# Optimization experiments

Hardware: AMD Instinct MI355X
Metric: run time of the kernel (lower is better)

Reference implementation:

```python
import jax, jax.numpy as jnp
import numpy as np

N = 100000
E = 1200000
F_IN = 128
HID = 32
HEADS = 4
OUT_HEADS = 1
N_CLASSES = 40
NEG_SLOPE = 0.2


def _glorot(key, shape):
    fan_in, fan_out = shape[0], shape[-1]
    lim = jnp.sqrt(6.0 / (fan_in + fan_out))
    return jax.random.uniform(key, shape, jnp.float32, -lim, lim)


def setup_inputs() -> dict:
    key = jax.random.key(0)
    ks = jax.random.split(key, 16)
    x = jax.random.normal(ks[0], (N, F_IN), jnp.float32)
    edge_index = jax.random.randint(ks[1], (2, E), 0, N, jnp.int32)
    # layer 0: F_IN -> HID per head, HEADS heads, concat
    W0 = _glorot(ks[2], (F_IN, HEADS * HID))
    a_src0 = _glorot(ks[3], (HEADS, HID))
    a_dst0 = _glorot(ks[4], (HEADS, HID))
    b0 = jnp.zeros((HEADS * HID,), jnp.float32)
    # layer 1: HEADS*HID -> HID per head, HEADS heads, concat
    W1 = _glorot(ks[5], (HEADS * HID, HEADS * HID))
    a_src1 = _glorot(ks[6], (HEADS, HID))
    a_dst1 = _glorot(ks[7], (HEADS, HID))
    b1 = jnp.zeros((HEADS * HID,), jnp.float32)
    # layer 2: HEADS*HID -> N_CLASSES, OUT_HEADS heads, concat=False (mean)
    W2 = _glorot(ks[8], (HEADS * HID, OUT_HEADS * N_CLASSES))
    a_src2 = _glorot(ks[9], (OUT_HEADS, N_CLASSES))
    a_dst2 = _glorot(ks[10], (OUT_HEADS, N_CLASSES))
    b2 = jnp.zeros((N_CLASSES,), jnp.float32)
    return dict(x=x, edge_index=edge_index,
                W0=W0, a_src0=a_src0, a_dst0=a_dst0, b0=b0,
                W1=W1, a_src1=a_src1, a_dst1=a_dst1, b1=b1,
                W2=W2, a_src2=a_src2, a_dst2=a_dst2, b2=b2)


def gat_conv(x, src, dst, W, a_src, a_dst, b, heads, ch, concat):
    n = x.shape[0]
    h = (x @ W).reshape(n, heads, ch)                      # [N,H,C]
    # per-node attention logits for source/target roles
    s_src = jnp.einsum('nhc,hc->nh', h, a_src)             # [N,H]
    s_dst = jnp.einsum('nhc,hc->nh', h, a_dst)             # [N,H]
    e = jax.nn.leaky_relu(s_src[src] + s_dst[dst], NEG_SLOPE)  # [E,H]
    # segment softmax over incoming edges of each target node
    emax = jax.ops.segment_max(e, dst, num_segments=n)
    ex = jnp.exp(e - emax[dst])
    denom = jax.ops.segment_sum(ex, dst, num_segments=n)
    alpha = ex / (denom[dst] + 1e-16)                       # [E,H]
    msg = h[src] * alpha[:, :, None]                        # [E,H,C]
    out = jax.ops.segment_sum(msg, dst, num_segments=n)     # [N,H,C]
    out = out.reshape(n, heads * ch) if concat else out.mean(axis=1)
    return out + b


def reference(x, edge_index, W0, a_src0, a_dst0, b0, W1, a_src1, a_dst1, b1,
              W2, a_src2, a_dst2, b2):
    # add self loops (PyG GATConv default)
    loops = jnp.arange(N, dtype=edge_index.dtype)
    src = jnp.concatenate([edge_index[0], loops])
    dst = jnp.concatenate([edge_index[1], loops])
    h = jax.nn.elu(gat_conv(x, src, dst, W0, a_src0, a_dst0, b0, HEADS, HID, True))
    h = jax.nn.elu(gat_conv(h, src, dst, W1, a_src1, a_dst1, b1, HEADS, HID, True))
    h = gat_conv(h, src, dst, W2, a_src2, a_dst2, b2, OUT_HEADS, N_CLASSES, False)
    return jax.nn.log_softmax(h, axis=1)
```

## Files before the change

kernel.cpp:

```cpp
#include <hip/hip_runtime.h>
#include <hip/hip_bf16.h>

#define FIN   128
#define HEADS 4
#define HID   32
#define NCLS  40
#define NEG_SLOPE 0.2f

#define BKT_SH 10
#define BKT    1024
#define NB_MAX 128
#define TILE_E 8192

typedef __bf16 bf16x8 __attribute__((ext_vector_type(8)));
typedef float  f32x4  __attribute__((ext_vector_type(4)));

__device__ inline unsigned short bf16_rne(float f) {
    unsigned u = __float_as_uint(f);
    return (unsigned short)((u + 0x7fffu + ((u >> 16) & 1u)) >> 16);
}
__device__ inline float bf16_to_f(unsigned short h) {
    return __uint_as_float(((unsigned)h) << 16);
}

__device__ inline void packW_dev(const float* __restrict__ W, unsigned short* __restrict__ Bhi,
                                 unsigned short* __restrict__ Blo, int NO, int NC, int idx) {
    int i = idx & 7;
    int rest = idx >> 3;
    int l = rest & 63;
    int rest2 = rest >> 6;
    int c = rest2 % NC;
    int t = rest2 / NC;
    int k   = t * 32 + (l >> 4) * 8 + i;
    int col = c * 16 + (l & 15);
    float val = (col < NO) ? W[(size_t)k * NO + col] : 0.f;
    unsigned short hi = bf16_rne(val);
    unsigned short lo = bf16_rne(val - bf16_to_f(hi));
    Bhi[idx] = hi;
    Blo[idx] = lo;
}

__device__ inline void packS_dev(const float* __restrict__ W, const float* __restrict__ asrc,
                                 const float* __restrict__ adst, unsigned short* __restrict__ Shi,
                                 unsigned short* __restrict__ Slo, int NO, int HH, int CH, int idx) {
    int i = idx & 7;
    int l = (idx >> 3) & 63;
    int t = idx >> 9;
    int k = t * 32 + (l >> 4) * 8 + i;
    int j = l & 15;
    float val = 0.f;
    if (j < 2 * HH) {
        int h = (j < HH) ? j : j - HH;
        const float* av = (j < HH) ? (asrc + h * CH) : (adst + h * CH);
        const float* wr = W + (size_t)k * NO + h * CH;
        for (int c = 0; c < CH; ++c) val += wr[c] * av[c];
    }
    unsigned short hi = bf16_rne(val);
    unsigned short lo = bf16_rne(val - bf16_to_f(hi));
    Shi[idx] = hi;
    Slo[idx] = lo;
}

__global__ __launch_bounds__(256) void packAll_k(
        const float* __restrict__ W0, const float* __restrict__ W1, const float* __restrict__ W2,
        const float* __restrict__ as0, const float* __restrict__ ad0,
        const float* __restrict__ as1, const float* __restrict__ ad1,
        const float* __restrict__ as2, const float* __restrict__ ad2,
        unsigned short* __restrict__ Bhi0, unsigned short* __restrict__ Blo0,
        unsigned short* __restrict__ Bhi1, unsigned short* __restrict__ Blo1,
        unsigned short* __restrict__ Bhi2, unsigned short* __restrict__ Blo2,
        unsigned short* __restrict__ Shi0, unsigned short* __restrict__ Slo0,
        unsigned short* __restrict__ Shi1, unsigned short* __restrict__ Slo1,
        unsigned short* __restrict__ Shi2, unsigned short* __restrict__ Slo2,
        int* __restrict__ cnt1) {
    int gid = blockIdx.x * 256 + threadIdx.x;
    if      (gid < 16384) packW_dev(W0, Bhi0, Blo0, 128, 8, gid);
    else if (gid < 32768) packW_dev(W1, Bhi1, Blo1, 128, 8, gid - 16384);
    else if (gid < 38912) packW_dev(W2, Bhi2, Blo2, NCLS, 3, gid - 32768);
    else if (gid < 40960) packS_dev(W0, as0, ad0, Shi0, Slo0, 128, 4, HID, gid - 38912);
    else if (gid < 43008) packS_dev(W1, as1, ad1, Shi1, Slo1, 128, 4, HID, gid - 40960);
    else if (gid < 45056) packS_dev(W2, as2, ad2, Shi2, Slo2, NCLS, 1, NCLS, gid - 43008);
    else if (gid < 45056 + NB_MAX) cnt1[gid - 45056] = 0;
}

template<int NC, int HH>
__global__ __launch_bounds__(256) void gemm_fused_k(
        const float* __restrict__ X, const unsigned short* __restrict__ Bhi,
        const unsigned short* __restrict__ Blo, const unsigned short* __restrict__ Shi,
        const unsigned short* __restrict__ Slo, unsigned short* __restrict__ Hbf,
        float* __restrict__ ssrc, float* __restrict__ sdst, int n, int NO) {
    int wave = threadIdx.x >> 6;
    int lane = threadIdx.x & 63;
    int rowbase = (blockIdx.x * 4 + wave) * 32;
    if (rowbase >= n) return;
    int r0 = lane & 15, kg = lane >> 4;

    f32x4 acc[2][NC];
    f32x4 accS[2];
#pragma unroll
    for (int rt = 0; rt < 2; ++rt) {
        accS[rt] = f32x4{0.f, 0.f, 0.f, 0.f};
#pragma unroll
        for (int c = 0; c < NC; ++c) acc[rt][c] = f32x4{0.f, 0.f, 0.f, 0.f};
    }

    for (int t = 0; t < 4; ++t) {
        union U { unsigned short u[8]; bf16x8 v; };
        U ah[2], al[2];
#pragma unroll
        for (int rt = 0; rt < 2; ++rt) {
            int row = min(rowbase + rt * 16 + r0, n - 1);
            const float* xp = X + (size_t)row * 128 + t * 32 + kg * 8;
            float4 xa = *reinterpret_cast<const float4*>(xp);
            float4 xb = *reinterpret_cast<const float4*>(xp + 4);
            float f[8] = {xa.x, xa.y, xa.z, xa.w, xb.x, xb.y, xb.z, xb.w};
#pragma unroll
            for (int i = 0; i < 8; ++i) {
                unsigned short h = bf16_rne(f[i]);
                ah[rt].u[i] = h;
                al[rt].u[i] = bf16_rne(f[i] - bf16_to_f(h));
            }
        }
#pragma unroll
        for (int c = 0; c < NC; ++c) {
            size_t boff = (((size_t)t * NC + c) * 64 + lane) * 8;
            bf16x8 bh = *reinterpret_cast<const bf16x8*>(Bhi + boff);
            bf16x8 bl = *reinterpret_cast<const bf16x8*>(Blo + boff);
#pragma unroll
            for (int rt = 0; rt < 2; ++rt) {
                acc[rt][c] = __builtin_amdgcn_mfma_f32_16x16x32_bf16(ah[rt].v, bh, acc[rt][c], 0, 0, 0);
                acc[rt][c] = __builtin_amdgcn_mfma_f32_16x16x32_bf16(al[rt].v, bh, acc[rt][c], 0, 0, 0);
                acc[rt][c] = __builtin_amdgcn_mfma_f32_16x16x32_bf16(ah[rt].v, bl, acc[rt][c], 0, 0, 0);
            }
        }
        {
            size_t soff = ((size_t)t * 64 + lane) * 8;
            bf16x8 sh = *reinterpret_cast<const bf16x8*>(Shi + soff);
            bf16x8 sl = *reinterpret_cast<const bf16x8*>(Slo + soff);
#pragma unroll
            for (int rt = 0; rt < 2; ++rt) {
                accS[rt] = __builtin_amdgcn_mfma_f32_16x16x32_bf16(ah[rt].v, sh, accS[rt], 0, 0, 0);
                accS[rt] = __builtin_amdgcn_mfma_f32_16x16x32_bf16(al[rt].v, sh, accS[rt], 0, 0, 0);
                accS[rt] = __builtin_amdgcn_mfma_f32_16x16x32_bf16(ah[rt].v, sl, accS[rt], 0, 0, 0);
            }
        }
    }

#pragma unroll
    for (int rt = 0; rt < 2; ++rt)
#pragma unroll
        for (int r = 0; r < 4; ++r) {
            int row = rowbase + rt * 16 + kg * 4 + r;
            if (row >= n) continue;
            if (HH == 4) {
                if (r0 < 4)      ssrc[(size_t)row * 4 + r0]       = accS[rt][r];
                else if (r0 < 8) sdst[(size_t)row * 4 + (r0 - 4)] = accS[rt][r];
            } else {
                if (r0 == 0)      ssrc[row] = accS[rt][r];
                else if (r0 == 1) sdst[row] = accS[rt][r];
            }
#pragma unroll
            for (int c = 0; c < NC; ++c) {
                int col = c * 16 + r0;
                if (col < NO)
                    Hbf[(size_t)row * NO + col] = bf16_rne(acc[rt][c][r]);
            }
        }
}

template<int NC, int HH, int OSTRIDE>
__global__ __launch_bounds__(256) void gemm_bf16s_k(
        const unsigned short* __restrict__ Xbf, const unsigned short* __restrict__ Bhi,
        const unsigned short* __restrict__ Blo, const unsigned short* __restrict__ Shi,
        const unsigned short* __restrict__ Slo, unsigned short* __restrict__ Hbf,
        float* __restrict__ ssrc, float* __restrict__ sdst, int n, int NO) {
    int wave = threadIdx.x >> 6;
    int lane = threadIdx.x & 63;
    int rowbase = (blockIdx.x * 4 + wave) * 32;
    if (rowbase >= n) return;
    int r0 = lane & 15, kg = lane >> 4;

    f32x4 acc[2][NC];
    f32x4 accS[2];
#pragma unroll
    for (int rt = 0; rt < 2; ++rt) {
        accS[rt] = f32x4{0.f, 0.f, 0.f, 0.f};
#pragma unroll
        for (int c = 0; c < NC; ++c) acc[rt][c] = f32x4{0.f, 0.f, 0.f, 0.f};
    }

    for (int t = 0; t < 4; ++t) {
        bf16x8 av[2];
#pragma unroll
        for (int rt = 0; rt < 2; ++rt) {
            int row = min(rowbase + rt * 16 + r0, n - 1);
            av[rt] = *reinterpret_cast<const bf16x8*>(Xbf + (size_t)row * 128 + t * 32 + kg * 8);
        }
#pragma unroll
        for (int c = 0; c < NC; ++c) {
            size_t boff = (((size_t)t * NC + c) * 64 + lane) * 8;
            bf16x8 bh = *reinterpret_cast<const bf16x8*>(Bhi + boff);
            bf16x8 bl = *reinterpret_cast<const bf16x8*>(Blo + boff);
#pragma unroll
            for (int rt = 0; rt < 2; ++rt) {
                acc[rt][c] = __builtin_amdgcn_mfma_f32_16x16x32_bf16(av[rt], bh, acc[rt][c], 0, 0, 0);
                acc[rt][c] = __builtin_amdgcn_mfma_f32_16x16x32_bf16(av[rt], bl, acc[rt][c], 0, 0, 0);
            }
        }
        {
            size_t soff = ((size_t)t * 64 + lane) * 8;
            bf16x8 sh = *reinterpret_cast<const bf16x8*>(Shi + soff);
            bf16x8 sl = *reinterpret_cast<const bf16x8*>(Slo + soff);
#pragma unroll
            for (int rt = 0; rt < 2; ++rt) {
                accS[rt] = __builtin_amdgcn_mfma_f32_16x16x32_bf16(av[rt], sh, accS[rt], 0, 0, 0);
                accS[rt] = __builtin_amdgcn_mfma_f32_16x16x32_bf16(av[rt], sl, accS[rt], 0, 0, 0);
            }
        }
    }

#pragma unroll
    for (int rt = 0; rt < 2; ++rt)
#pragma unroll
        for (int r = 0; r < 4; ++r) {
            int row = rowbase + rt * 16 + kg * 4 + r;
            if (row >= n) continue;
            if (HH == 4) {
                if (r0 < 4)      ssrc[(size_t)row * 4 + r0]       = accS[rt][r];
                else if (r0 < 8) sdst[(size_t)row * 4 + (r0 - 4)] = accS[rt][r];
            } else {
                if (r0 == 0)      ssrc[row] = accS[rt][r];
                else if (r0 == 1) sdst[row] = accS[rt][r];
            }
#pragma unroll
            for (int c = 0; c < NC; ++c) {
                int col = c * 16 + r0;
                if (col < NO)
                    Hbf[(size_t)row * OSTRIDE + col] = bf16_rne(acc[rt][c][r]);
            }
        }
}

__global__ __launch_bounds__(256) void histA_k(const int* __restrict__ ei, int E, int Etot,
                                               int nb, int* __restrict__ cnt1) {
    __shared__ int h[NB_MAX];
    for (int i = threadIdx.x; i < nb; i += 256) h[i] = 0;
    __syncthreads();
    int base = blockIdx.x * TILE_E;
    int lim = min(base + TILE_E, Etot);
    for (int e = base + threadIdx.x; e < lim; e += 256) {
        int d = (e < E) ? ei[E + e] : e - E;
        atomicAdd(&h[d >> BKT_SH], 1);
    }
    __syncthreads();
    for (int i = threadIdx.x; i < nb; i += 256)
        if (h[i]) atomicAdd(&cnt1[i], h[i]);
}

__global__ void scanB_k(const int* __restrict__ cnt1, int* __restrict__ bbase,
                        int* __restrict__ gcur1, int nb) {
    __shared__ int tmp[128];
    int l = threadIdx.x;
    int v = (l < nb) ? cnt1[l] : 0;
    tmp[l] = v;
    __syncthreads();
    for (int off = 1; off < 128; off <<= 1) {
        int t = (l >= off) ? tmp[l - off] : 0;
        __syncthreads();
        tmp[l] += t;
        __syncthreads();
    }
    if (l < nb) { int ex = tmp[l] - v; bbase[l] = ex; gcur1[l] = ex; }
    if (l == 0) bbase[nb] = tmp[127];
}

__global__ __launch_bounds__(256) void placeA_k(const int* __restrict__ ei, int E, int Etot,
                                                int nb, int* __restrict__ gcur1,
                                                unsigned* __restrict__ pairs) {
    __shared__ int h[NB_MAX];
    __shared__ int cur[NB_MAX];
    for (int i = threadIdx.x; i < nb; i += 256) h[i] = 0;
    __syncthreads();
    int base = blockIdx.x * TILE_E;
    int lim = min(base + TILE_E, Etot);
    for (int e = base + threadIdx.x; e < lim; e += 256) {
        int d = (e < E) ? ei[E + e] : e - E;
        atomicAdd(&h[d >> BKT_SH], 1);
    }
    __syncthreads();
    for (int i = threadIdx.x; i < nb; i += 256)
        cur[i] = h[i] ? atomicAdd(&gcur1[i], h[i]) : 0;
    __syncthreads();
    for (int e = base + threadIdx.x; e < lim; e += 256) {
        int s, d;
        if (e < E) { s = ei[e]; d = ei[E + e]; } else { s = d = e - E; }
        int p = atomicAdd(&cur[d >> BKT_SH], 1);
        pairs[p] = ((unsigned)s << BKT_SH) | (unsigned)(d & (BKT - 1));
    }
}

__global__ __launch_bounds__(256) void buildcsr_k(const unsigned* __restrict__ pairs,
                                                  const int* __restrict__ bbase,
                                                  int* __restrict__ rowptr,
                                                  int* __restrict__ cols,
                                                  int n, int etot) {
    __shared__ int cnt[BKT];
    __shared__ int part[256];
    int b = blockIdx.x;
    int d0 = b << BKT_SH;
    int nd = min(BKT, n - d0);
    int rbeg = bbase[b], rend = bbase[b + 1];
    for (int i = threadIdx.x; i < nd; i += 256) cnt[i] = 0;
    __syncthreads();
    for (int i = rbeg + threadIdx.x; i < rend; i += 256)
        atomicAdd(&cnt[pairs[i] & (BKT - 1)], 1);
    __syncthreads();

    int t = threadIdx.x;
    int i4 = t * 4;
    int myv[4];
    int s0 = 0;
#pragma unroll
    for (int j = 0; j < 4; ++j) { myv[j] = (i4 + j < nd) ? cnt[i4 + j] : 0; s0 += myv[j]; }
    part[t] = s0;
    __syncthreads();
    for (int off = 1; off < 256; off <<= 1) {
        int tv = (t >= off) ? part[t - off] : 0;
        __syncthreads();
        part[t] += tv;
        __syncthreads();
    }
    int run = rbeg + part[t] - s0;
#pragma unroll
    for (int j = 0; j < 4; ++j) {
        if (i4 + j < nd) {
            rowptr[d0 + i4 + j] = run;
            cnt[i4 + j] = run;
            run += myv[j];
        }
    }
    if (b == 0 && t == 0) rowptr[n] = etot;
    __syncthreads();
    for (int i = rbeg + threadIdx.x; i < rend; i += 256) {
        unsigned p = pairs[i];
        int pos = atomicAdd(&cnt[p & (BKT - 1)], 1);
        cols[pos] = (int)(p >> BKT_SH);
    }
}

__global__ __launch_bounds__(256) void gat128_k(
        const int* __restrict__ rp, const int* __restrict__ cols,
        const unsigned short* __restrict__ Hbf, const float* __restrict__ ssrc,
        const float* __restrict__ sdst, const float* __restrict__ bias,
        unsigned short* __restrict__ outbf, int n) {
    int d = (blockIdx.x * 256 + threadIdx.x) >> 4;
    if (d >= n) return;
    int l = threadIdx.x & 15;
    int head = l >> 2;
    int sub  = l & 3;
    int beg = rp[d], end = rp[d + 1];

    float sdh = sdst[(size_t)d * 4 + head];

    float m = -1e30f, den = 0.f;
    for (int i = beg + sub; i < end; i += 4) {
        int s = cols[i];
        float v = ssrc[(size_t)s * 4 + head] + sdh;
        v = (v >= 0.f) ? v : NEG_SLOPE * v;
        float nm = fmaxf(m, v);
        den = den * __expf(m - nm) + __expf(v - nm);
        m = nm;
    }
#pragma unroll
    for (int off = 1; off <= 2; off <<= 1) {
        float om = __shfl_xor(m, off, 64);
        float od = __shfl_xor(den, off, 64);
        float nm = fmaxf(m, om);
        den = den * __expf(m - nm) + od * __expf(om - nm);
        m = nm;
    }
    float r = 1.f / (den + 1e-16f);

    float4 a0 = {0.f, 0.f, 0.f, 0.f}, a1 = {0.f, 0.f, 0.f, 0.f};
    float4 c0 = {0.f, 0.f, 0.f, 0.f}, c1 = {0.f, 0.f, 0.f, 0.f};

    auto proc = [&](int i, float4& p0, float4& p1) {
        int s = cols[i];
        float v = ssrc[(size_t)s * 4 + head] + sdh;
        v = (v >= 0.f) ? v : NEG_SLOPE * v;
        float a = __expf(v - m);
        const unsigned short* hp = Hbf + (size_t)s * 128 + l * 8;
        uint4 q = *reinterpret_cast<const uint4*>(hp);
        p0.x += a * __uint_as_float(q.x << 16);
        p0.y += a * __uint_as_float(q.x & 0xffff0000u);
        p0.z += a * __uint_as_float(q.y << 16);
        p0.w += a * __uint_as_float(q.y & 0xffff0000u);
        p1.x += a * __uint_as_float(q.z << 16);
        p1.y += a * __uint_as_float(q.z & 0xffff0000u);
        p1.z += a * __uint_as_float(q.w << 16);
        p1.w += a * __uint_as_float(q.w & 0xffff0000u);
    };

    int i = beg;
    int rem = (end - beg) & 3;
    if (rem & 1) { proc(i, a0, a1); ++i; }
    if (rem & 2) { proc(i, a0, a1); proc(i + 1, c0, c1); i += 2; }
    for (; i < end; i += 4) {
        int s0 = cols[i], s1 = cols[i + 1], s2 = cols[i + 2], s3 = cols[i + 3];
        float w0 = ssrc[(size_t)s0 * 4 + head] + sdh;
        float w1 = ssrc[(size_t)s1 * 4 + head] + sdh;
        float w2 = ssrc[(size_t)s2 * 4 + head] + sdh;
        float w3 = ssrc[(size_t)s3 * 4 + head] + sdh;
        uint4 q0 = *reinterpret_cast<const uint4*>(Hbf + (size_t)s0 * 128 + l * 8);
        uint4 q1 = *reinterpret_cast<const uint4*>(Hbf + (size_t)s1 * 128 + l * 8);
        uint4 q2 = *reinterpret_cast<const uint4*>(Hbf + (size_t)s2 * 128 + l * 8);
        uint4 q3 = *reinterpret_cast<const uint4*>(Hbf + (size_t)s3 * 128 + l * 8);
        w0 = (w0 >= 0.f) ? w0 : NEG_SLOPE * w0;
        w1 = (w1 >= 0.f) ? w1 : NEG_SLOPE * w1;
        w2 = (w2 >= 0.f) ? w2 : NEG_SLOPE * w2;
        w3 = (w3 >= 0.f) ? w3 : NEG_SLOPE * w3;
        float e0 = __expf(w0 - m), e1 = __expf(w1 - m);
        float e2 = __expf(w2 - m), e3 = __expf(w3 - m);
        a0.x += e0 * __uint_as_float(q0.x << 16);
        a0.y += e0 * __uint_as_float(q0.x & 0xffff0000u);
        a0.z += e0 * __uint_as_float(q0.y << 16);
        a0.w += e0 * __uint_as_float(q0.y & 0xffff0000u);
        a1.x += e0 * __uint_as_float(q0.z << 16);
        a1.y += e0 * __uint_as_float(q0.z & 0xffff0000u);
        a1.z += e0 * __uint_as_float(q0.w << 16);
        a1.w += e0 * __uint_as_float(q0.w & 0xffff0000u);
        c0.x += e1 * __uint_as_float(q1.x << 16);
        c0.y += e1 * __uint_as_float(q1.x & 0xffff0000u);
        c0.z += e1 * __uint_as_float(q1.y << 16);
        c0.w += e1 * __uint_as_float(q1.y & 0xffff0000u);
        c1.x += e1 * __uint_as_float(q1.z << 16);
        c1.y += e1 * __uint_as_float(q1.z & 0xffff0000u);
        c1.z += e1 * __uint_as_float(q1.w << 16);
        c1.w += e1 * __uint_as_float(q1.w & 0xffff0000u);
        a0.x += e2 * __uint_as_float(q2.x << 16);
        a0.y += e2 * __uint_as_float(q2.x & 0xffff0000u);
        a0.z += e2 * __uint_as_float(q2.y << 16);
        a0.w += e2 * __uint_as_float(q2.y & 0xffff0000u);
        a1.x += e2 * __uint_as_float(q2.z << 16);
        a1.y += e2 * __uint_as_float(q2.z & 0xffff0000u);
        a1.z += e2 * __uint_as_float(q2.w << 16);
        a1.w += e2 * __uint_as_float(q2.w & 0xffff0000u);
        c0.x += e3 * __uint_as_float(q3.x << 16);
        c0.y += e3 * __uint_as_float(q3.x & 0xffff0000u);
        c0.z += e3 * __uint_as_float(q3.y << 16);
        c0.w += e3 * __uint_as_float(q3.y & 0xffff0000u);
        c1.x += e3 * __uint_as_float(q3.z << 16);
        c1.y += e3 * __uint_as_float(q3.z & 0xffff0000u);
        c1.z += e3 * __uint_as_float(q3.w << 16);
        c1.w += e3 * __uint_as_float(q3.w & 0xffff0000u);
    }
    a0.x += c0.x; a0.y += c0.y; a0.z += c0.z; a0.w += c0.w;
    a1.x += c1.x; a1.y += c1.y; a1.z += c1.z; a1.w += c1.w;

    float4 b0 = *reinterpret_cast<const float4*>(bias + l * 8);
    float4 b1 = *reinterpret_cast<const float4*>(bias + l * 8 + 4);
    float4 v0, v1;
    v0.x = a0.x * r + b0.x; v0.y = a0.y * r + b0.y;
    v0.z = a0.z * r + b0.z; v0.w = a0.w * r + b0.w;
    v1.x = a1.x * r + b1.x; v1.y = a1.y * r + b1.y;
    v1.z = a1.z * r + b1.z; v1.w = a1.w * r + b1.w;
    v0.x = (v0.x > 0.f) ? v0.x : expm1f(v0.x);
    v0.y = (v0.y > 0.f) ? v0.y : expm1f(v0.y);
    v0.z = (v0.z > 0.f) ? v0.z : expm1f(v0.z);
    v0.w = (v0.w > 0.f) ? v0.w : expm1f(v0.w);
    v1.x = (v1.x > 0.f) ? v1.x : expm1f(v1.x);
    v1.y = (v1.y > 0.f) ? v1.y : expm1f(v1.y);
    v1.z = (v1.z > 0.f) ? v1.z : expm1f(v1.z);
    v1.w = (v1.w > 0.f) ? v1.w : expm1f(v1.w);

    uint4 u;
    u.x = (unsigned)bf16_rne(v0.x) | ((unsigned)bf16_rne(v0.y) << 16);
    u.y = (unsigned)bf16_rne(v0.z) | ((unsigned)bf16_rne(v0.w) << 16);
    u.z = (unsigned)bf16_rne(v1.x) | ((unsigned)bf16_rne(v1.y) << 16);
    u.w = (unsigned)bf16_rne(v1.z) | ((unsigned)bf16_rne(v1.w) << 16);
    *reinterpret_cast<uint4*>(outbf + (size_t)d * 128 + l * 8) = u;
}

__global__ __launch_bounds__(256) void gat40_k(
        const int* __restrict__ rp, const int* __restrict__ cols,
        const unsigned short* __restrict__ Hbf, const float* __restrict__ ssrc,
        const float* __restrict__ sdst, const float* __restrict__ b2,
        float* __restrict__ out, int n) {
    int d = (blockIdx.x * 256 + threadIdx.x) >> 4;
    if (d >= n) return;
    int l = threadIdx.x & 15;
    int beg = rp[d], end = rp[d + 1];
    float sd = sdst[d];

    float m = -1e30f, den = 0.f;
    for (int i = beg + l; i < end; i += 16) {
        int s = cols[i];
        float v = ssrc[s] + sd;
        v = (v >= 0.f) ? v : NEG_SLOPE * v;
        float nm = fmaxf(m, v);
        den = den * __expf(m - nm) + __expf(v - nm);
        m = nm;
    }
#pragma unroll
    for (int off = 1; off <= 8; off <<= 1) {
        float om = __shfl_xor(m, off, 64);
        float od = __shfl_xor(den, off, 64);
        float nm = fmaxf(m, om);
        den = den * __expf(m - nm) + od * __expf(om - nm);
        m = nm;
    }
    float r = 1.f / (den + 1e-16f);

    float4 acc = {0.f, 0.f, 0.f, 0.f};
    float4 acc2 = {0.f, 0.f, 0.f, 0.f};
    auto proc = [&](int i, float4& p) {
        int s = cols[i];
        float v = ssrc[s] + sd;
        v = (v >= 0.f) ? v : NEG_SLOPE * v;
        float a = __expf(v - m);
        uint2 q = *reinterpret_cast<const uint2*>(Hbf + (size_t)s * 64 + l * 4);
        p.x += a * __uint_as_float(q.x << 16);
        p.y += a * __uint_as_float(q.x & 0xffff0000u);
        p.z += a * __uint_as_float(q.y << 16);
        p.w += a * __uint_as_float(q.y & 0xffff0000u);
    };
    int i = beg;
    int rem = (end - beg) & 3;
    if (rem & 1) { proc(i, acc); ++i; }
    if (rem & 2) { proc(i, acc); proc(i + 1, acc2); i += 2; }
    for (; i < end; i += 4) {
        int s0 = cols[i], s1 = cols[i + 1], s2 = cols[i + 2], s3 = cols[i + 3];
        float w0 = ssrc[s0] + sd, w1 = ssrc[s1] + sd;
        float w2 = ssrc[s2] + sd, w3 = ssrc[s3] + sd;
        uint2 q0 = *reinterpret_cast<const uint2*>(Hbf + (size_t)s0 * 64 + l * 4);
        uint2 q1 = *reinterpret_cast<const uint2*>(Hbf + (size_t)s1 * 64 + l * 4);
        uint2 q2 = *reinterpret_cast<const uint2*>(Hbf + (size_t)s2 * 64 + l * 4);
        uint2 q3 = *reinterpret_cast<const uint2*>(Hbf + (size_t)s3 * 64 + l * 4);
        w0 = (w0 >= 0.f) ? w0 : NEG_SLOPE * w0;
        w1 = (w1 >= 0.f) ? w1 : NEG_SLOPE * w1;
        w2 = (w2 >= 0.f) ? w2 : NEG_SLOPE * w2;
        w3 = (w3 >= 0.f) ? w3 : NEG_SLOPE * w3;
        float e0 = __expf(w0 - m), e1 = __expf(w1 - m);
        float e2 = __expf(w2 - m), e3 = __expf(w3 - m);
        acc.x += e0 * __uint_as_float(q0.x << 16);
        acc.y += e0 * __uint_as_float(q0.x & 0xffff0000u);
        acc.z += e0 * __uint_as_float(q0.y << 16);
        acc.w += e0 * __uint_as_float(q0.y & 0xffff0000u);
        acc2.x += e1 * __uint_as_float(q1.x << 16);
        acc2.y += e1 * __uint_as_float(q1.x & 0xffff0000u);
        acc2.z += e1 * __uint_as_float(q1.y << 16);
        acc2.w += e1 * __uint_as_float(q1.y & 0xffff0000u);
        acc.x += e2 * __uint_as_float(q2.x << 16);
        acc.y += e2 * __uint_as_float(q2.x & 0xffff0000u);
        acc.z += e2 * __uint_as_float(q2.y << 16);
        acc.w += e2 * __uint_as_float(q2.y & 0xffff0000u);
        acc2.x += e3 * __uint_as_float(q3.x << 16);
        acc2.y += e3 * __uint_as_float(q3.x & 0xffff0000u);
        acc2.z += e3 * __uint_as_float(q3.y << 16);
        acc2.w += e3 * __uint_as_float(q3.y & 0xffff0000u);
    }
    acc.x += acc2.x; acc.y += acc2.y; acc.z += acc2.z; acc.w += acc2.w;

    float4 v4 = {0.f, 0.f, 0.f, 0.f};
    float mm = -1e30f;
    if (l < 10) {
        float4 b = *reinterpret_cast<const float4*>(b2 + l * 4);
        v4.x = acc.x * r + b.x; v4.y = acc.y * r + b.y;
        v4.z = acc.z * r + b.z; v4.w = acc.w * r + b.w;
        mm = fmaxf(fmaxf(v4.x, v4.y), fmaxf(v4.z, v4.w));
    }
    for (int off = 8; off > 0; off >>= 1) mm = fmaxf(mm, __shfl_xor(mm, off, 16));
    float ss = 0.f;
    if (l < 10)
        ss = __expf(v4.x - mm) + __expf(v4.y - mm) + __expf(v4.z - mm) + __expf(v4.w - mm);
    for (int off = 8; off > 0; off >>= 1) ss += __shfl_xor(ss, off, 16);
    float lse = mm + logf(ss);
    if (l < 10) {
        float4 o;
        o.x = v4.x - lse; o.y = v4.y - lse; o.z = v4.z - lse; o.w = v4.w - lse;
        *reinterpret_cast<float4*>(out + (size_t)d * 40 + l * 4) = o;
    }
}

static inline dim3 g1(long t) { return dim3((unsigned)((t + 255) / 256)); }

extern "C" void kernel_launch(void* const* d_in, const int* in_sizes, int n_in,
                              void* d_out, int out_size, void* d_ws, size_t ws_size,
                              hipStream_t stream) {
    const float* x      = (const float*)d_in[0];
    const int*   ei     = (const int*)d_in[1];
    const float* W0     = (const float*)d_in[2];
    const float* a_src0 = (const float*)d_in[3];
    const float* a_dst0 = (const float*)d_in[4];
    const float* b0     = (const float*)d_in[5];
    const float* W1     = (const float*)d_in[6];
    const float* a_src1 = (const float*)d_in[7];
    const float* a_dst1 = (const float*)d_in[8];
    const float* b1     = (const float*)d_in[9];
    const float* W2     = (const float*)d_in[10];
    const float* a_src2 = (const float*)d_in[11];
    const float* a_dst2 = (const float*)d_in[12];
    const float* b2     = (const float*)d_in[13];

    const int N    = in_sizes[0] / FIN;
    const int E    = in_sizes[1] / 2;
    const int Etot = E + N;
    const int NB   = (N + BKT - 1) / BKT;

    float* ws = (float*)d_ws;
    size_t o = 0;
    unsigned short* Hbf = (unsigned short*)(ws + o); o += (size_t)N * FIN / 2;
    unsigned short* Obf = (unsigned short*)(ws + o); o += (size_t)N * FIN / 2;
    float* ssrcA = ws + o; o += (size_t)N * HEADS;
    float* sdstA = ws + o; o += (size_t)N * HEADS;
    float* ssrcB = ws + o; o += (size_t)N * HEADS;
    float* sdstB = ws + o; o += (size_t)N * HEADS;
    int* cnt1   = (int*)(ws + o); o += NB_MAX;
    int* bbase  = (int*)(ws + o); o += NB_MAX + 2;
    int* gcur1  = (int*)(ws + o); o += NB_MAX;
    int* rowptr = (int*)(ws + o); o += N + 1;
    int* cols   = (int*)(ws + o); o += Etot;
    unsigned* pairs = (unsigned*)(ws + o); o += Etot;
    unsigned short* Bhi0 = (unsigned short*)(ws + o); o += 4 * 8 * 64 * 8 / 2;
    unsigned short* Blo0 = (unsigned short*)(ws + o); o += 4 * 8 * 64 * 8 / 2;
    unsigned short* Bhi1 = (unsigned short*)(ws + o); o += 4 * 8 * 64 * 8 / 2;
    unsigned short* Blo1 = (unsigned short*)(ws + o); o += 4 * 8 * 64 * 8 / 2;
    unsigned short* Bhi2 = (unsigned short*)(ws + o); o += 4 * 3 * 64 * 8 / 2;
    unsigned short* Blo2 = (unsigned short*)(ws + o); o += 4 * 3 * 64 * 8 / 2;
    unsigned short* Shi0 = (unsigned short*)(ws + o); o += 4 * 64 * 8 / 2;
    unsigned short* Slo0 = (unsigned short*)(ws + o); o += 4 * 64 * 8 / 2;
    unsigned short* Shi1 = (unsigned short*)(ws + o); o += 4 * 64 * 8 / 2;
    unsigned short* Slo1 = (unsigned short*)(ws + o); o += 4 * 64 * 8 / 2;
    unsigned short* Shi2 = (unsigned short*)(ws + o); o += 4 * 64 * 8 / 2;
    unsigned short* Slo2 = (unsigned short*)(ws + o); o += 4 * 64 * 8 / 2;

    const int gemmBlocks = (N + 127) / 128;
    const int grpBlocks  = (N * 16 + 255) / 256;
    const int eTiles     = (Etot + TILE_E - 1) / TILE_E;

    packAll_k<<<g1(45056 + NB_MAX), 256, 0, stream>>>(
        W0, W1, W2, a_src0, a_dst0, a_src1, a_dst1, a_src2, a_dst2,
        Bhi0, Blo0, Bhi1, Blo1, Bhi2, Blo2,
        Shi0, Slo0, Shi1, Slo1, Shi2, Slo2, cnt1);
    histA_k<<<eTiles, 256, 0, stream>>>(ei, E, Etot, NB, cnt1);
    scanB_k<<<1, 128, 0, stream>>>(cnt1, bbase, gcur1, NB);
    placeA_k<<<eTiles, 256, 0, stream>>>(ei, E, Etot, NB, gcur1, pairs);
    buildcsr_k<<<NB, 256, 0, stream>>>(pairs, bbase, rowptr, cols, N, Etot);

    gemm_fused_k<8, 4><<<gemmBlocks, 256, 0, stream>>>(x, Bhi0, Blo0, Shi0, Slo0, Hbf, ssrcA, sdstA, N, 128);
    gat128_k<<<grpBlocks, 256, 0, stream>>>(rowptr, cols, Hbf, ssrcA, sdstA, b0, Obf, N);

    gemm_bf16s_k<8, 4, 128><<<gemmBlocks, 256, 0, stream>>>(Obf, Bhi1, Blo1, Shi1, Slo1, Hbf, ssrcB, sdstB, N, 128);
    gat128_k<<<grpBlocks, 256, 0, stream>>>(rowptr, cols, Hbf, ssrcB, sdstB, b1, Obf, N);

    gemm_bf16s_k<3, 1, 64><<<gemmBlocks, 256, 0, stream>>>(Obf, Bhi2, Blo2, Shi2, Slo2, Hbf, ssrcA, sdstA, N, NCLS);
    gat40_k<<<grpBlocks, 256, 0, stream>>>(rowptr, cols, Hbf, ssrcA, sdstA, b2, (float*)d_out, N);
}
```

Baseline: 331.7 us.

## Drop softmax max pass in GAT aggregation and split layer-2 features compactly

Removes the first pass over each node's incoming edges, which computed the running max and denominator. The exponentials are now taken unshifted and the denominator is accumulated in the same loop as the weighted feature sum, so each edge list is read once instead of twice. The layer-2 projected features are also stored as a dense 32-column array plus an 8-column side array instead of a padded 64-column row, which cuts gather traffic. Skipping the max subtraction risks exp overflow or precision loss if the attention logits get large.

```diff
diff --git a/kernel.cpp b/kernel.cpp
--- a/kernel.cpp
+++ b/kernel.cpp
@@ -168,11 +168,12 @@
         }
 }
 
-template<int NC, int HH, int OSTRIDE>
+template<int NC, int HH, bool SPLIT>
 __global__ __launch_bounds__(256) void gemm_bf16s_k(
         const unsigned short* __restrict__ Xbf, const unsigned short* __restrict__ Bhi,
         const unsigned short* __restrict__ Blo, const unsigned short* __restrict__ Shi,
         const unsigned short* __restrict__ Slo, unsigned short* __restrict__ Hbf,
+        unsigned short* __restrict__ H8,
         float* __restrict__ ssrc, float* __restrict__ sdst, int n, int NO) {
     int wave = threadIdx.x >> 6;
     int lane = threadIdx.x & 63;
@@ -235,8 +236,15 @@
 #pragma unroll
             for (int c = 0; c < NC; ++c) {
                 int col = c * 16 + r0;
-                if (col < NO)
-                    Hbf[(size_t)row * OSTRIDE + col] = bf16_rne(acc[rt][c][r]);
+                if (col < NO) {
+                    unsigned short b = bf16_rne(acc[rt][c][r]);
+                    if (!SPLIT) {
+                        Hbf[(size_t)row * 128 + col] = b;
+                    } else {
+                        if (col < 32) Hbf[(size_t)row * 32 + col] = b;
+                        else          H8[(size_t)row * 8 + (col - 32)] = b;
+                    }
+                }
             }
         }
 }
@@ -357,38 +365,20 @@
     if (d >= n) return;
     int l = threadIdx.x & 15;
     int head = l >> 2;
-    int sub  = l & 3;
     int beg = rp[d], end = rp[d + 1];
 
     float sdh = sdst[(size_t)d * 4 + head];
-
-    float m = -1e30f, den = 0.f;
-    for (int i = beg + sub; i < end; i += 4) {
-        int s = cols[i];
-        float v = ssrc[(size_t)s * 4 + head] + sdh;
-        v = (v >= 0.f) ? v : NEG_SLOPE * v;
-        float nm = fmaxf(m, v);
-        den = den * __expf(m - nm) + __expf(v - nm);
-        m = nm;
-    }
-#pragma unroll
-    for (int off = 1; off <= 2; off <<= 1) {
-        float om = __shfl_xor(m, off, 64);
-        float od = __shfl_xor(den, off, 64);
-        float nm = fmaxf(m, om);
-        den = den * __expf(m - nm) + od * __expf(om - nm);
-        m = nm;
-    }
-    float r = 1.f / (den + 1e-16f);
 
     float4 a0 = {0.f, 0.f, 0.f, 0.f}, a1 = {0.f, 0.f, 0.f, 0.f};
     float4 c0 = {0.f, 0.f, 0.f, 0.f}, c1 = {0.f, 0.f, 0.f, 0.f};
+    float den = 0.f;
 
     auto proc = [&](int i, float4& p0, float4& p1) {
         int s = cols[i];
         float v = ssrc[(size_t)s * 4 + head] + sdh;
         v = (v >= 0.f) ? v : NEG_SLOPE * v;
-        float a = __expf(v - m);
+        float a = __expf(v);
+        den += a;
         const unsigned short* hp = Hbf + (size_t)s * 128 + l * 8;
         uint4 q = *reinterpret_cast<const uint4*>(hp);
         p0.x += a * __uint_as_float(q.x << 16);
@@ -419,8 +409,9 @@
         w1 = (w1 >= 0.f) ? w1 : NEG_SLOPE * w1;
         w2 = (w2 >= 0.f) ? w2 : NEG_SLOPE * w2;
         w3 = (w3 >= 0.f) ? w3 : NEG_SLOPE * w3;
-        float e0 = __expf(w0 - m), e1 = __expf(w1 - m);
-        float e2 = __expf(w2 - m), e3 = __expf(w3 - m);
+        float e0 = __expf(w0), e1 = __expf(w1);
+        float e2 = __expf(w2), e3 = __expf(w3);
+        den += e0 + e1 + e2 + e3;
         a0.x += e0 * __uint_as_float(q0.x << 16);
         a0.y += e0 * __uint_as_float(q0.x & 0xffff0000u);
         a0.z += e0 * __uint_as_float(q0.y << 16);
@@ -457,6 +448,7 @@
     a0.x += c0.x; a0.y += c0.y; a0.z += c0.z; a0.w += c0.w;
     a1.x += c1.x; a1.y += c1.y; a1.z += c1.z; a1.w += c1.w;
 
+    float r = 1.f / (den + 1e-16f);
     float4 b0 = *reinterpret_cast<const float4*>(bias + l * 8);
     float4 b1 = *reinterpret_cast<const float4*>(bias + l * 8 + 4);
     float4 v0, v1;
@@ -483,42 +475,32 @@
 
 __global__ __launch_bounds__(256) void gat40_k(
         const int* __restrict__ rp, const int* __restrict__ cols,
-        const unsigned short* __restrict__ Hbf, const float* __restrict__ ssrc,
-        const float* __restrict__ sdst, const float* __restrict__ b2,
-        float* __restrict__ out, int n) {
+        const unsigned short* __restrict__ H32, const unsigned short* __restrict__ H8,
+        const float* __restrict__ ssrc, const float* __restrict__ sdst,
+        const float* __restrict__ b2, float* __restrict__ out, int n) {
     int d = (blockIdx.x * 256 + threadIdx.x) >> 4;
     if (d >= n) return;
     int l = threadIdx.x & 15;
     int beg = rp[d], end = rp[d + 1];
     float sd = sdst[d];
 
-    float m = -1e30f, den = 0.f;
-    for (int i = beg + l; i < end; i += 16) {
-        int s = cols[i];
-        float v = ssrc[s] + sd;
-        v = (v >= 0.f) ? v : NEG_SLOPE * v;
-        float nm = fmaxf(m, v);
-        den = den * __expf(m - nm) + __expf(v - nm);
-        m = nm;
-    }
-#pragma unroll
-    for (int off = 1; off <= 8; off <<= 1) {
-        float om = __shfl_xor(m, off, 64);
-        float od = __shfl_xor(den, off, 64);
-        float nm = fmaxf(m, om);
-        den = den * __expf(m - nm) + od * __expf(om - nm);
-        m = nm;
-    }
-    float r = 1.f / (den + 1e-16f);
+    bool lo32 = (l < 8);
+    int o32 = l * 4;
+    int o8  = ((l >= 8 && l < 10) ? (l - 8) : 0) * 4;
 
     float4 acc = {0.f, 0.f, 0.f, 0.f};
     float4 acc2 = {0.f, 0.f, 0.f, 0.f};
+    float den = 0.f;
+
     auto proc = [&](int i, float4& p) {
         int s = cols[i];
         float v = ssrc[s] + sd;
         v = (v >= 0.f) ? v : NEG_SLOPE * v;
-        float a = __expf(v - m);
-        uint2 q = *reinterpret_cast<const uint2*>(Hbf + (size_t)s * 64 + l * 4);
+        float a = __expf(v);
+        den += a;
+        const unsigned short* hp = lo32 ? (H32 + (size_t)s * 32 + o32)
+                                        : (H8  + (size_t)s * 8  + o8);
+        uint2 q = *reinterpret_cast<const uint2*>(hp);
         p.x += a * __uint_as_float(q.x << 16);
         p.y += a * __uint_as_float(q.x & 0xffff0000u);
         p.z += a * __uint_as_float(q.y << 16);
@@ -532,16 +514,21 @@
         int s0 = cols[i], s1 = cols[i + 1], s2 = cols[i + 2], s3 = cols[i + 3];
         float w0 = ssrc[s0] + sd, w1 = ssrc[s1] + sd;
         float w2 = ssrc[s2] + sd, w3 = ssrc[s3] + sd;
-        uint2 q0 = *reinterpret_cast<const uint2*>(Hbf + (size_t)s0 * 64 + l * 4);
-        uint2 q1 = *reinterpret_cast<const uint2*>(Hbf + (size_t)s1 * 64 + l * 4);
-        uint2 q2 = *reinterpret_cast<const uint2*>(Hbf + (size_t)s2 * 64 + l * 4);
-        uint2 q3 = *reinterpret_cast<const uint2*>(Hbf + (size_t)s3 * 64 + l * 4);
+        const unsigned short* p0 = lo32 ? (H32 + (size_t)s0 * 32 + o32) : (H8 + (size_t)s0 * 8 + o8);
+        const unsigned short* p1 = lo32 ? (H32 + (size_t)s1 * 32 + o32) : (H8 + (size_t)s1 * 8 + o8);
+        const unsigned short* p2 = lo32 ? (H32 + (size_t)s2 * 32 + o32) : (H8 + (size_t)s2 * 8 + o8);
+        const unsigned short* p3 = lo32 ? (H32 + (size_t)s3 * 32 + o32) : (H8 + (size_t)s3 * 8 + o8);
+        uint2 q0 = *reinterpret_cast<const uint2*>(p0);
+        uint2 q1 = *reinterpret_cast<const uint2*>(p1);
+        uint2 q2 = *reinterpret_cast<const uint2*>(p2);
+        uint2 q3 = *reinterpret_cast<const uint2*>(p3);
         w0 = (w0 >= 0.f) ? w0 : NEG_SLOPE * w0;
         w1 = (w1 >= 0.f) ? w1 : NEG_SLOPE * w1;
         w2 = (w2 >= 0.f) ? w2 : NEG_SLOPE * w2;
         w3 = (w3 >= 0.f) ? w3 : NEG_SLOPE * w3;
-        float e0 = __expf(w0 - m), e1 = __expf(w1 - m);
-        float e2 = __expf(w2 - m), e3 = __expf(w3 - m);
+        float e0 = __expf(w0), e1 = __expf(w1);
+        float e2 = __expf(w2), e3 = __expf(w3);
+        den += e0 + e1 + e2 + e3;
         acc.x += e0 * __uint_as_float(q0.x << 16);
         acc.y += e0 * __uint_as_float(q0.x & 0xffff0000u);
         acc.z += e0 * __uint_as_float(q0.y << 16);
@@ -561,6 +548,7 @@
     }
     acc.x += acc2.x; acc.y += acc2.y; acc.z += acc2.z; acc.w += acc2.w;
 
+    float r = 1.f / (den + 1e-16f);
     float4 v4 = {0.f, 0.f, 0.f, 0.f};
     float mm = -1e30f;
     if (l < 10) {
@@ -611,6 +599,7 @@
     size_t o = 0;
     unsigned short* Hbf = (unsigned short*)(ws + o); o += (size_t)N * FIN / 2;
     unsigned short* Obf = (unsigned short*)(ws + o); o += (size_t)N * FIN / 2;
+    unsigned short* H8  = (unsigned short*)(ws + o); o += (size_t)N * 4;
     float* ssrcA = ws + o; o += (size_t)N * HEADS;
     float* sdstA = ws + o; o += (size_t)N * HEADS;
     float* ssrcB = ws + o; o += (size_t)N * HEADS;
@@ -650,9 +639,9 @@
     gemm_fused_k<8, 4><<<gemmBlocks, 256, 0, stream>>>(x, Bhi0, Blo0, Shi0, Slo0, Hbf, ssrcA, sdstA, N, 128);
     gat128_k<<<grpBlocks, 256, 0, stream>>>(rowptr, cols, Hbf, ssrcA, sdstA, b0, Obf, N);
 
-    gemm_bf16s_k<8, 4, 128><<<gemmBlocks, 256, 0, stream>>>(Obf, Bhi1, Blo1, Shi1, Slo1, Hbf, ssrcB, sdstB, N, 128);
+    gemm_bf16s_k<8, 4, false><<<gemmBlocks, 256, 0, stream>>>(Obf, Bhi1, Blo1, Shi1, Slo1, Hbf, nullptr, ssrcB, sdstB, N, 128);
     gat128_k<<<grpBlocks, 256, 0, stream>>>(rowptr, cols, Hbf, ssrcB, sdstB, b1, Obf, N);
 
-    gemm_bf16s_k<3, 1, 64><<<gemmBlocks, 256, 0, stream>>>(Obf, Bhi2, Blo2, Shi2, Slo2, Hbf, ssrcA, sdstA, N, NCLS);
-    gat40_k<<<grpBlocks, 256, 0, stream>>>(rowptr, cols, Hbf, ssrcA, sdstA, b2, (float*)d_out, N);
-}
+    gemm_bf16s_k<3, 1, true><<<gemmBlocks, 256, 0, stream>>>(Obf, Bhi2, Blo2, Shi2, Slo2, Hbf, H8, ssrcA, sdstA, N, NCLS);
+    gat40_k<<<grpBlocks, 256, 0, stream>>>(rowptr, cols, Hbf, H8, ssrcA, sdstA, b2, (float*)d_out, N);
+}
```

Result: faster. 311.7 us (-6.0%).
